# Optimization experiments

Measured on AMD Instinct MI355X. Metric: run time of the kernel, lower is better.

Reference implementation:

```python
import jax, jax.numpy as jnp
import numpy as np

SEQ_LEN, BATCH, IN_SIZE = 512, 1024, 3
HID, HID_FC, OUT = 512, 512, 1
HORIZON = 96


def gru_cell(x, h, w_ih, w_hh, b_ih, b_hh):
    # PyTorch GRU cell math. x: [B, in], h: [B, H], w_ih: [3H, in], w_hh: [3H, H]
    gi = x @ w_ih.T + b_ih
    gh = h @ w_hh.T + b_hh
    i_r, i_z, i_n = jnp.split(gi, 3, axis=-1)
    h_r, h_z, h_n = jnp.split(gh, 3, axis=-1)
    r = jax.nn.sigmoid(i_r + h_r)
    z = jax.nn.sigmoid(i_z + h_z)
    n = jnp.tanh(i_n + r * h_n)
    return (1.0 - z) * n + z * h


def setup_inputs() -> dict:
    key = jax.random.key(0)
    ks = jax.random.split(key, 16)
    s_in = 1.0 / np.sqrt(HID)
    inp = {
        'src': jax.random.normal(ks[0], (SEQ_LEN, BATCH, IN_SIZE), dtype=jnp.float32),
        'enc_wih': jax.random.uniform(ks[1], (3 * HID, IN_SIZE), minval=-s_in, maxval=s_in),
        'enc_whh': jax.random.uniform(ks[2], (3 * HID, HID), minval=-s_in, maxval=s_in),
        'enc_bih': jax.random.uniform(ks[3], (3 * HID,), minval=-s_in, maxval=s_in),
        'enc_bhh': jax.random.uniform(ks[4], (3 * HID,), minval=-s_in, maxval=s_in),
        'dec_wih': jax.random.uniform(ks[5], (3 * HID, OUT), minval=-s_in, maxval=s_in),
        'dec_whh': jax.random.uniform(ks[6], (3 * HID, HID), minval=-s_in, maxval=s_in),
        'dec_bih': jax.random.uniform(ks[7], (3 * HID,), minval=-s_in, maxval=s_in),
        'dec_bhh': jax.random.uniform(ks[8], (3 * HID,), minval=-s_in, maxval=s_in),
        'w1': jax.random.uniform(ks[9], (HID_FC, HID), minval=-s_in, maxval=s_in),
        'b1': jax.random.uniform(ks[10], (HID_FC,), minval=-s_in, maxval=s_in),
        'w2': jax.random.uniform(ks[11], (OUT, HID_FC), minval=-1.0 / np.sqrt(HID_FC), maxval=1.0 / np.sqrt(HID_FC)),
        'b2': jax.random.uniform(ks[12], (OUT,), minval=-1.0 / np.sqrt(HID_FC), maxval=1.0 / np.sqrt(HID_FC)),
        'horizon': HORIZON,
    }
    return inp


def reference(src, enc_wih, enc_whh, enc_bih, enc_bhh,
              dec_wih, dec_whh, dec_bih, dec_bhh,
              w1, b1, w2, b2, horizon):
    B = src.shape[1]
    h0 = jnp.zeros((B, HID), dtype=src.dtype)

    # Encoder: run GRU over time; only final hidden state is used.
    def enc_step(h, x_t):
        return gru_cell(x_t, h, enc_wih, enc_whh, enc_bih, enc_bhh), None
    h, _ = jax.lax.scan(enc_step, h0, src)

    dec_in0 = src[-1, :, 0:1]  # [B, 1]

    def dec_step(carry, _):
        dec_in, h = carry
        h = gru_cell(dec_in, h, dec_wih, dec_whh, dec_bih, dec_bhh)
        y = jax.nn.relu(h @ w1.T + b1) @ w2.T + b2  # [B, 1]
        return (y, h), y
    _, outputs = jax.lax.scan(dec_step, (dec_in0, h), None, length=horizon)
    return outputs  # [horizon, B, 1]
```

## Files before the change

kernel.cpp:

```cpp
#include <hip/hip_runtime.h>

typedef __bf16 bf16x8 __attribute__((ext_vector_type(8)));
typedef float f32x4 __attribute__((ext_vector_type(4)));

#define HID 512
#define BATCH 1024
#define SEQL 512
#define NWG 256
#define NTHR 512

#define OFF_ENH 0u
#define OFF_ENL 1572864u
#define OFF_DEH 3145728u
#define OFF_DEL 4718592u
#define OFF_W1H 6291456u
#define OFF_W1L 6815744u
#define OFF_HP0 7340032u
#define OFF_HP1 9437184u
#define OFF_FC1 11534336u
#define OFF_BAR 13631488u
#define WS_NEED 13635584u

#define LDS_LO 32768
#define SWZ(row, cb) (((row) << 10) + ((cb) ^ (((row) & 7) << 4)))

__device__ __forceinline__ f32x4 mfma16(bf16x8 a, bf16x8 b, f32x4 c) {
  return __builtin_amdgcn_mfma_f32_16x16x32_bf16(a, b, c, 0, 0, 0);
}
__device__ __forceinline__ float sig_(float x) { return 1.0f / (1.0f + __expf(-x)); }
__device__ __forceinline__ float tanh_(float x) { return 1.0f - 2.0f / (__expf(2.0f * x) + 1.0f); }

__device__ __forceinline__ unsigned long long ald64(const void* p) {
  return __hip_atomic_load((const unsigned long long*)p, __ATOMIC_RELAXED,
                           __HIP_MEMORY_SCOPE_AGENT);
}
__device__ __forceinline__ void ast32(void* p, unsigned v) {
  __hip_atomic_store((unsigned*)p, v, __ATOMIC_RELAXED, __HIP_MEMORY_SCOPE_AGENT);
}
__device__ __forceinline__ void astf(void* p, float v) {
  __hip_atomic_store((float*)p, v, __ATOMIC_RELAXED, __HIP_MEMORY_SCOPE_AGENT);
}

__global__ void split_w(const float* __restrict__ a, __bf16* __restrict__ hi,
                        __bf16* __restrict__ lo, int n) {
  int i = blockIdx.x * blockDim.x + threadIdx.x;
  if (i < n) {
    float v = a[i];
    __bf16 h = (__bf16)v;
    hi[i] = h;
    lo[i] = (__bf16)(v - (float)h);
  }
}

__device__ __forceinline__ void gbar(unsigned* cnt, unsigned target) {
  __syncthreads();
  if (threadIdx.x == 0) {
    __hip_atomic_fetch_add(cnt, 1u, __ATOMIC_RELAXED, __HIP_MEMORY_SCOPE_AGENT);
    int i = 0;
    while (__hip_atomic_load(cnt, __ATOMIC_RELAXED, __HIP_MEMORY_SCOPE_AGENT) < target) {
      __builtin_amdgcn_s_sleep(2);
      if (++i >= 30000) break;
    }
  }
  __syncthreads();
  __builtin_amdgcn_sched_barrier(0);
}

__device__ __forceinline__ void stage_h32(char* sm, const unsigned* hsrc, int row0, int tid) {
  const int cp = tid & 255;
  const int rh = (tid >> 8) << 4;
  const unsigned long long* src =
      (const unsigned long long*)hsrc + ((size_t)(row0 + rh) << 8) + cp;
  unsigned long long b[16];
#pragma unroll
  for (int j = 0; j < 16; ++j) b[j] = ald64(src + (size_t)j * 256);
#pragma unroll
  for (int j = 0; j < 16; ++j) {
    const int row = rh + j;
    const unsigned p0 = (unsigned)b[j];
    const unsigned p1 = (unsigned)(b[j] >> 32);
    const unsigned hw = (p0 & 0xffffu) | (p1 << 16);
    const unsigned lw = (p0 >> 16) | (p1 & 0xffff0000u);
    const int sa = SWZ(row, cp << 2);
    *(unsigned*)(sm + sa) = hw;
    *(unsigned*)(sm + LDS_LO + sa) = lw;
  }
}

__device__ __forceinline__ void gh3(const char* sm, int rl, int kbb,
                                    const __bf16* __restrict__ Bh,
                                    const __bf16* __restrict__ Bl,
                                    const int (&boff)[3], f32x4 (&acc)[3]) {
#pragma unroll 4
  for (int kc = 0; kc < 16; ++kc) {
    const int sa = SWZ(rl, (kc << 6) + kbb);
    bf16x8 ah = *(const bf16x8*)(sm + sa);
    bf16x8 al = *(const bf16x8*)(sm + LDS_LO + sa);
    const int ko = kc << 5;
#pragma unroll
    for (int f = 0; f < 3; ++f) {
      bf16x8 bh = *(const bf16x8*)(Bh + boff[f] + ko);
      bf16x8 bl = *(const bf16x8*)(Bl + boff[f] + ko);
      acc[f] = mfma16(ah, bh, acc[f]);
      acc[f] = mfma16(al, bh, acc[f]);
      acc[f] = mfma16(ah, bl, acc[f]);
    }
  }
}

__device__ __forceinline__ void gh1(const char* sm, int rl, int kbb,
                                    const __bf16* __restrict__ Bh,
                                    const __bf16* __restrict__ Bl, int boff, f32x4& acc) {
#pragma unroll 4
  for (int kc = 0; kc < 16; ++kc) {
    const int sa = SWZ(rl, (kc << 6) + kbb);
    bf16x8 ah = *(const bf16x8*)(sm + sa);
    bf16x8 al = *(const bf16x8*)(sm + LDS_LO + sa);
    const int ko = kc << 5;
    bf16x8 bh = *(const bf16x8*)(Bh + boff + ko);
    bf16x8 bl = *(const bf16x8*)(Bl + boff + ko);
    acc = mfma16(ah, bh, acc);
    acc = mfma16(al, bh, acc);
    acc = mfma16(ah, bl, acc);
  }
}

__global__ void __launch_bounds__(NTHR, 2) seq2seq_main(
    const float* __restrict__ src, const float* __restrict__ enc_wih,
    const float* __restrict__ enc_bih, const float* __restrict__ enc_bhh,
    const float* __restrict__ dec_wih, const float* __restrict__ dec_bih,
    const float* __restrict__ dec_bhh, const float* __restrict__ b1,
    const float* __restrict__ w2, const float* __restrict__ b2,
    const int* __restrict__ hor, float* __restrict__ out, char* __restrict__ ws) {
  __shared__ f32x4 smv[4096];
  char* sm = (char*)smv;
  float* yb = (float*)sm;

  const __bf16* ench_hi = (const __bf16*)(ws + OFF_ENH);
  const __bf16* ench_lo = (const __bf16*)(ws + OFF_ENL);
  const __bf16* dech_hi = (const __bf16*)(ws + OFF_DEH);
  const __bf16* dech_lo = (const __bf16*)(ws + OFF_DEL);
  const __bf16* w1h = (const __bf16*)(ws + OFF_W1H);
  const __bf16* w1l = (const __bf16*)(ws + OFF_W1L);
  unsigned* hp0 = (unsigned*)(ws + OFF_HP0);
  unsigned* hp1 = (unsigned*)(ws + OFF_HP1);
  float* fc1 = (float*)(ws + OFF_FC1);

  const int bid = blockIdx.x;
  const int G = bid >> 3;
  const int ct = bid & 7;
  const int tid = threadIdx.x;
  const int wv = tid >> 6;
  const int lane = tid & 63;
  const int lan15 = lane & 15;
  const int crow = (lane >> 4) << 2;
  const int kbe = (lane >> 4) << 3;
  const int kbb = kbe << 1;
  const int wr = wv & 1;
  const int wc = wv >> 1;
  const int rl = (wr << 4) + lan15;
  const int row0 = G << 5;
  const int cg = (ct << 6) + (wc << 4) + lan15;

  unsigned* cnt = (unsigned*)(ws + OFF_BAR) + (G << 5);

  int boff[3];
#pragma unroll
  for (int g = 0; g < 3; ++g) boff[g] = ((g << 9) + cg) * HID + kbe;
  const int boff_fc = cg * HID + kbe;

  float wE[3][3], biE[3], bhE[3];
#pragma unroll
  for (int g = 0; g < 3; ++g) {
    const int j = (g << 9) + cg;
    wE[g][0] = enc_wih[j * 3 + 0];
    wE[g][1] = enc_wih[j * 3 + 1];
    wE[g][2] = enc_wih[j * 3 + 2];
    biE[g] = enc_bih[j];
    bhE[g] = enc_bhh[j];
  }

  const f32x4 zf = {0.0f, 0.0f, 0.0f, 0.0f};
  float hpv[4] = {0.f, 0.f, 0.f, 0.f};

  for (int t = 0; t < SEQL; ++t) {
    f32x4 acc[3];
#pragma unroll
    for (int f = 0; f < 3; ++f) acc[f] = zf;

    if (t != 0) {
      stage_h32(sm, (t & 1) ? hp1 : hp0, row0, tid);
      __syncthreads();
      gh3(sm, rl, kbb, ench_hi, ench_lo, boff, acc);
    }

    unsigned* hn = ((t + 1) & 1) ? hp1 : hp0;
#pragma unroll
    for (int reg = 0; reg < 4; ++reg) {
      const int row = row0 + (wr << 4) + crow + reg;
      const float* xp = src + ((size_t)t * BATCH + row) * 3;
      const float x0 = xp[0], x1 = xp[1], x2 = xp[2];
      const float gir = fmaf(x0, wE[0][0], fmaf(x1, wE[0][1], fmaf(x2, wE[0][2], biE[0])));
      const float giz = fmaf(x0, wE[1][0], fmaf(x1, wE[1][1], fmaf(x2, wE[1][2], biE[1])));
      const float gin = fmaf(x0, wE[2][0], fmaf(x1, wE[2][1], fmaf(x2, wE[2][2], biE[2])));
      const float rg = sig_(gir + acc[0][reg] + bhE[0]);
      const float zg = sig_(giz + acc[1][reg] + bhE[1]);
      const float ng = tanh_(gin + rg * (acc[2][reg] + bhE[2]));
      const float hv = fmaf(zg, hpv[reg] - ng, ng);
      hpv[reg] = hv;
      const __bf16 hb = (__bf16)hv;
      const __bf16 lb = (__bf16)(hv - (float)hb);
      const unsigned pw = (unsigned)__builtin_bit_cast(unsigned short, hb) |
                          ((unsigned)__builtin_bit_cast(unsigned short, lb) << 16);
      ast32(hn + (size_t)row * HID + cg, pw);
    }
    gbar(cnt, 8u * (unsigned)(t + 1));
  }

  float wD[3], biD[3], bhD[3];
#pragma unroll
  for (int g = 0; g < 3; ++g) {
    const int j = (g << 9) + cg;
    wD[g] = dec_wih[j];
    biD[g] = dec_bih[j];
    bhD[g] = dec_bhh[j];
  }
  const float b1c = b1[cg];
  const float b2v = b2[0];
  float w2p0[4], w2p1[4];
#pragma unroll
  for (int j = 0; j < 4; ++j) {
    w2p0[j] = w2[2 * (lane + j * 64)];
    w2p1[j] = w2[2 * (lane + j * 64) + 1];
  }
  int H = hor[0];
  if (H < 1 || H > 96) H = 96;

  for (int t = 0; t < H; ++t) {
    float din[4];
    if (t == 0) {
#pragma unroll
      for (int reg = 0; reg < 4; ++reg) {
        const int row = row0 + (wr << 4) + crow + reg;
        din[reg] = src[((size_t)(SEQL - 1) * BATCH + row) * 3];
      }
    } else {
#pragma unroll
      for (int rr = 0; rr < 4; ++rr) {
        const int row = row0 + (wv << 2) + rr;
        const unsigned long long* fp = (const unsigned long long*)fc1 + ((size_t)row << 8);
        float s = 0.0f;
#pragma unroll
        for (int j = 0; j < 4; ++j) {
          const unsigned long long w = ald64(fp + lane + (j << 6));
          const float f0 = __builtin_bit_cast(float, (unsigned)(w & 0xffffffffULL));
          const float f1 = __builtin_bit_cast(float, (unsigned)(w >> 32));
          s = fmaf(f0, w2p0[j], fmaf(f1, w2p1[j], s));
        }
#pragma unroll
        for (int off = 1; off < 64; off <<= 1) s += __shfl_xor(s, off, 64);
        if (lane == 0) yb[(wv << 2) + rr] = s + b2v;
      }
      __syncthreads();
      if (ct == 0 && tid < 32) out[(size_t)(t - 1) * BATCH + row0 + tid] = yb[tid];
#pragma unroll
      for (int reg = 0; reg < 4; ++reg) din[reg] = yb[(wr << 4) + crow + reg];
      __syncthreads();
    }

    {
      stage_h32(sm, (t & 1) ? hp1 : hp0, row0, tid);
      __syncthreads();
      f32x4 acc[3];
#pragma unroll
      for (int f = 0; f < 3; ++f) acc[f] = zf;
      gh3(sm, rl, kbb, dech_hi, dech_lo, boff, acc);

      unsigned* hn = ((t + 1) & 1) ? hp1 : hp0;
#pragma unroll
      for (int reg = 0; reg < 4; ++reg) {
        const int row = row0 + (wr << 4) + crow + reg;
        const float d = din[reg];
        const float rg = sig_(fmaf(d, wD[0], biD[0]) + acc[0][reg] + bhD[0]);
        const float zg = sig_(fmaf(d, wD[1], biD[1]) + acc[1][reg] + bhD[1]);
        const float ng = tanh_(fmaf(d, wD[2], biD[2]) + rg * (acc[2][reg] + bhD[2]));
        const float hv = fmaf(zg, hpv[reg] - ng, ng);
        hpv[reg] = hv;
        const __bf16 hb = (__bf16)hv;
        const __bf16 lb = (__bf16)(hv - (float)hb);
        const unsigned pw = (unsigned)__builtin_bit_cast(unsigned short, hb) |
                            ((unsigned)__builtin_bit_cast(unsigned short, lb) << 16);
        ast32(hn + (size_t)row * HID + cg, pw);
      }
    }
    gbar(cnt, 8u * (unsigned)(SEQL + 2 * t + 1));

    {
      stage_h32(sm, ((t + 1) & 1) ? hp1 : hp0, row0, tid);
      __syncthreads();
      f32x4 fa = zf;
      gh1(sm, rl, kbb, w1h, w1l, boff_fc, fa);
#pragma unroll
      for (int reg = 0; reg < 4; ++reg) {
        const int row = row0 + (wr << 4) + crow + reg;
        astf(&fc1[(size_t)row * HID + cg], fmaxf(fa[reg] + b1c, 0.0f));
      }
    }
    gbar(cnt, 8u * (unsigned)(SEQL + 2 * t + 2));
  }

  if (ct == 0) {
#pragma unroll
    for (int rr = 0; rr < 4; ++rr) {
      const int row = row0 + (wv << 2) + rr;
      const unsigned long long* fp = (const unsigned long long*)fc1 + ((size_t)row << 8);
      float s = 0.0f;
#pragma unroll
      for (int j = 0; j < 4; ++j) {
        const unsigned long long w = ald64(fp + lane + (j << 6));
        const float f0 = __builtin_bit_cast(float, (unsigned)(w & 0xffffffffULL));
        const float f1 = __builtin_bit_cast(float, (unsigned)(w >> 32));
        s = fmaf(f0, w2p0[j], fmaf(f1, w2p1[j], s));
      }
#pragma unroll
      for (int off = 1; off < 64; off <<= 1) s += __shfl_xor(s, off, 64);
      if (lane == 0) yb[(wv << 2) + rr] = s + b2v;
    }
    __syncthreads();
    if (tid < 32) out[(size_t)(H - 1) * BATCH + row0 + tid] = yb[tid];
  }
}

extern "C" void kernel_launch(void* const* d_in, const int* in_sizes, int n_in,
                              void* d_out, int out_size, void* d_ws, size_t ws_size,
                              hipStream_t stream) {
  if (ws_size < WS_NEED) return;

  const float* src = (const float*)d_in[0];
  const float* enc_wih = (const float*)d_in[1];
  const float* enc_whh = (const float*)d_in[2];
  const float* enc_bih = (const float*)d_in[3];
  const float* enc_bhh = (const float*)d_in[4];
  const float* dec_wih = (const float*)d_in[5];
  const float* dec_whh = (const float*)d_in[6];
  const float* dec_bih = (const float*)d_in[7];
  const float* dec_bhh = (const float*)d_in[8];
  const float* w1 = (const float*)d_in[9];
  const float* b1 = (const float*)d_in[10];
  const float* w2 = (const float*)d_in[11];
  const float* b2 = (const float*)d_in[12];
  const int* hor = (const int*)d_in[13];
  float* out = (float*)d_out;
  char* ws = (char*)d_ws;

  hipMemsetAsync(ws + OFF_BAR, 0, 4096, stream);

  split_w<<<dim3(3072), dim3(256), 0, stream>>>(enc_whh, (__bf16*)(ws + OFF_ENH),
                                                (__bf16*)(ws + OFF_ENL), 786432);
  split_w<<<dim3(3072), dim3(256), 0, stream>>>(dec_whh, (__bf16*)(ws + OFF_DEH),
                                                (__bf16*)(ws + OFF_DEL), 786432);
  split_w<<<dim3(1024), dim3(256), 0, stream>>>(w1, (__bf16*)(ws + OFF_W1H),
                                                (__bf16*)(ws + OFF_W1L), 262144);

  void* args[] = {&src, &enc_wih, &enc_bih, &enc_bhh, &dec_wih, &dec_bih, &dec_bhh,
                  &b1, &w2, &b2, &hor, &out, &ws};
  hipLaunchCooperativeKernel((void*)seq2seq_main, dim3(NWG), dim3(NTHR), args, 0, stream);
}
```

Before: 16.29 ms.

## Assign row groups and column tiles per XCD so barrier groups share an XCD

At kernel start, each workgroup reads its hardware XCD id and claims a slot from a per-XCD counter. The slot sets the (column tile, row group) pair, so that the 8 column tiles of one row group and its per-group barrier land on the same XCD and keep L2 locality for the h exchange. Workgroups that do not get a slot fall back to a CAS search over unclaimed pairs. A grid-wide wait with a timeout sits between the two phases. The encoder also issues its src input loads before the h staging and MFMA work so their latency overlaps. The change adds startup atomics and a spin, and relies on XCC_ID placement.

```diff
diff --git a/kernel.cpp b/kernel.cpp
--- a/kernel.cpp
+++ b/kernel.cpp
@@ -19,7 +19,8 @@
 #define OFF_HP1 9437184u
 #define OFF_FC1 11534336u
 #define OFF_BAR 13631488u
-#define WS_NEED 13635584u
+#define OFF_ASN 13635584u
+#define WS_NEED 13639680u
 
 #define LDS_LO 32768
 #define SWZ(row, cb) (((row) << 10) + ((cb) ^ (((row) & 7) << 4)))
@@ -135,6 +136,7 @@
   __shared__ f32x4 smv[4096];
   char* sm = (char*)smv;
   float* yb = (float*)sm;
+  int* s_pair = (int*)sm;
 
   const __bf16* ench_hi = (const __bf16*)(ws + OFF_ENH);
   const __bf16* ench_lo = (const __bf16*)(ws + OFF_ENL);
@@ -145,11 +147,53 @@
   unsigned* hp0 = (unsigned*)(ws + OFF_HP0);
   unsigned* hp1 = (unsigned*)(ws + OFF_HP1);
   float* fc1 = (float*)(ws + OFF_FC1);
+  unsigned* xcd_cnt = (unsigned*)(ws + OFF_ASN);
+  unsigned* root = (unsigned*)(ws + OFF_ASN + 512);
+  unsigned* taken = (unsigned*)(ws + OFF_ASN + 1024);
 
   const int bid = blockIdx.x;
-  const int G = bid >> 3;
-  const int ct = bid & 7;
   const int tid = threadIdx.x;
+
+  if (tid == 0) {
+    int xcd;
+    asm volatile("s_getreg_b32 %0, hwreg(HW_REG_XCC_ID)" : "=s"(xcd));
+    xcd &= 7;
+    const unsigned slot = __hip_atomic_fetch_add(&xcd_cnt[xcd * 16], 1u, __ATOMIC_RELAXED,
+                                                 __HIP_MEMORY_SCOPE_AGENT);
+    int p = -1;
+    if (slot < 32u) {
+      p = xcd * 32 + (int)slot;
+      __hip_atomic_store(&taken[p], 1u, __ATOMIC_RELAXED, __HIP_MEMORY_SCOPE_AGENT);
+    }
+    __hip_atomic_fetch_add(root, 1u, __ATOMIC_RELEASE, __HIP_MEMORY_SCOPE_AGENT);
+    int i = 0;
+    while (__hip_atomic_load(root, __ATOMIC_ACQUIRE, __HIP_MEMORY_SCOPE_AGENT) < NWG) {
+      __builtin_amdgcn_s_sleep(2);
+      if (++i >= 30000) break;
+    }
+    if (p < 0) {
+      for (int k = 0; k < 256; ++k) {
+        const int j = (bid + k) & 255;
+        if (__hip_atomic_load(&taken[j], __ATOMIC_RELAXED, __HIP_MEMORY_SCOPE_AGENT) == 0u) {
+          unsigned exp = 0u;
+          if (__hip_atomic_compare_exchange_strong(&taken[j], &exp, 1u, __ATOMIC_ACQ_REL,
+                                                   __ATOMIC_RELAXED,
+                                                   __HIP_MEMORY_SCOPE_AGENT)) {
+            p = j;
+            break;
+          }
+        }
+      }
+    }
+    if (p < 0) p = ((bid & 7) << 5) | (bid >> 3);
+    *s_pair = p;
+  }
+  __syncthreads();
+  const int pr = *s_pair;
+  __syncthreads();
+  const int ct = pr >> 5;
+  const int G = pr & 31;
+
   const int wv = tid >> 6;
   const int lane = tid & 63;
   const int lan15 = lane & 15;
@@ -184,6 +228,16 @@
   float hpv[4] = {0.f, 0.f, 0.f, 0.f};
 
   for (int t = 0; t < SEQL; ++t) {
+    float xv[4][3];
+#pragma unroll
+    for (int reg = 0; reg < 4; ++reg) {
+      const int row = row0 + (wr << 4) + crow + reg;
+      const float* xp = src + ((size_t)t * BATCH + row) * 3;
+      xv[reg][0] = xp[0];
+      xv[reg][1] = xp[1];
+      xv[reg][2] = xp[2];
+    }
+
     f32x4 acc[3];
 #pragma unroll
     for (int f = 0; f < 3; ++f) acc[f] = zf;
@@ -198,8 +252,7 @@
 #pragma unroll
     for (int reg = 0; reg < 4; ++reg) {
       const int row = row0 + (wr << 4) + crow + reg;
-      const float* xp = src + ((size_t)t * BATCH + row) * 3;
-      const float x0 = xp[0], x1 = xp[1], x2 = xp[2];
+      const float x0 = xv[reg][0], x1 = xv[reg][1], x2 = xv[reg][2];
       const float gir = fmaf(x0, wE[0][0], fmaf(x1, wE[0][1], fmaf(x2, wE[0][2], biE[0])));
       const float giz = fmaf(x0, wE[1][0], fmaf(x1, wE[1][1], fmaf(x2, wE[1][2], biE[1])));
       const float gin = fmaf(x0, wE[2][0], fmaf(x1, wE[2][1], fmaf(x2, wE[2][2], biE[2])));
@@ -353,7 +406,7 @@
   float* out = (float*)d_out;
   char* ws = (char*)d_ws;
 
-  hipMemsetAsync(ws + OFF_BAR, 0, 4096, stream);
+  hipMemsetAsync(ws + OFF_BAR, 0, 8192, stream);
 
   split_w<<<dim3(3072), dim3(256), 0, stream>>>(enc_whh, (__bf16*)(ws + OFF_ENH),
                                                 (__bf16*)(ws + OFF_ENL), 786432);
```

Measured after the change: 16.02 ms. About the same (-1.7%).

## Split work across 512 smaller workgroups of 16 batch rows each

Applied to the files above, without the earlier changes.

Changes the persistent grid from 256 workgroups of 512 threads handling 32 batch rows each to 512 workgroups of 256 threads handling 16 rows, halving LDS staging per group and raising occupancy bounds. It also hoists the per-step input loads ahead of the recurrent matmul so their latency overlaps it. The cooperative launch is replaced with a plain launch, so co-residency of all 512 groups for the spin barrier is no longer guaranteed and the barrier has a timeout break. Each group now redundantly streams the full weight slices for half as many rows, doubling weight reads per row.

```diff
diff --git a/kernel.cpp b/kernel.cpp
--- a/kernel.cpp
+++ b/kernel.cpp
@@ -6,8 +6,8 @@
 #define HID 512
 #define BATCH 1024
 #define SEQL 512
-#define NWG 256
-#define NTHR 512
+#define NWG 512
+#define NTHR 256
 
 #define OFF_ENH 0u
 #define OFF_ENL 1572864u
@@ -19,9 +19,9 @@
 #define OFF_HP1 9437184u
 #define OFF_FC1 11534336u
 #define OFF_BAR 13631488u
-#define WS_NEED 13635584u
-
-#define LDS_LO 32768
+#define WS_NEED 13639680u
+
+#define LDS_LO 16384
 #define SWZ(row, cb) (((row) << 10) + ((cb) ^ (((row) & 7) << 4)))
 
 __device__ __forceinline__ f32x4 mfma16(bf16x8 a, bf16x8 b, f32x4 c) {
@@ -66,22 +66,18 @@
   __builtin_amdgcn_sched_barrier(0);
 }
 
-__device__ __forceinline__ void stage_h32(char* sm, const unsigned* hsrc, int row0, int tid) {
-  const int cp = tid & 255;
-  const int rh = (tid >> 8) << 4;
-  const unsigned long long* src =
-      (const unsigned long long*)hsrc + ((size_t)(row0 + rh) << 8) + cp;
+__device__ __forceinline__ void stage_h16(char* sm, const unsigned* hsrc, int row0, int tid) {
+  const unsigned long long* src = (const unsigned long long*)hsrc + ((size_t)row0 << 8) + tid;
   unsigned long long b[16];
 #pragma unroll
   for (int j = 0; j < 16; ++j) b[j] = ald64(src + (size_t)j * 256);
 #pragma unroll
   for (int j = 0; j < 16; ++j) {
-    const int row = rh + j;
     const unsigned p0 = (unsigned)b[j];
     const unsigned p1 = (unsigned)(b[j] >> 32);
     const unsigned hw = (p0 & 0xffffu) | (p1 << 16);
     const unsigned lw = (p0 >> 16) | (p1 & 0xffff0000u);
-    const int sa = SWZ(row, cp << 2);
+    const int sa = SWZ(j, tid << 2);
     *(unsigned*)(sm + sa) = hw;
     *(unsigned*)(sm + LDS_LO + sa) = lw;
   }
@@ -125,14 +121,14 @@
   }
 }
 
-__global__ void __launch_bounds__(NTHR, 2) seq2seq_main(
+__global__ void __launch_bounds__(NTHR, 4) seq2seq_main(
     const float* __restrict__ src, const float* __restrict__ enc_wih,
     const float* __restrict__ enc_bih, const float* __restrict__ enc_bhh,
     const float* __restrict__ dec_wih, const float* __restrict__ dec_bih,
     const float* __restrict__ dec_bhh, const float* __restrict__ b1,
     const float* __restrict__ w2, const float* __restrict__ b2,
     const int* __restrict__ hor, float* __restrict__ out, char* __restrict__ ws) {
-  __shared__ f32x4 smv[4096];
+  __shared__ f32x4 smv[2048];
   char* sm = (char*)smv;
   float* yb = (float*)sm;
 
@@ -156,11 +152,9 @@
   const int crow = (lane >> 4) << 2;
   const int kbe = (lane >> 4) << 3;
   const int kbb = kbe << 1;
-  const int wr = wv & 1;
-  const int wc = wv >> 1;
-  const int rl = (wr << 4) + lan15;
-  const int row0 = G << 5;
-  const int cg = (ct << 6) + (wc << 4) + lan15;
+  const int rl = lan15;
+  const int row0 = G << 4;
+  const int cg = (ct << 6) + (wv << 4) + lan15;
 
   unsigned* cnt = (unsigned*)(ws + OFF_BAR) + (G << 5);
 
@@ -184,12 +178,22 @@
   float hpv[4] = {0.f, 0.f, 0.f, 0.f};
 
   for (int t = 0; t < SEQL; ++t) {
+    float xv[4][3];
+#pragma unroll
+    for (int reg = 0; reg < 4; ++reg) {
+      const int row = row0 + crow + reg;
+      const float* xp = src + ((size_t)t * BATCH + row) * 3;
+      xv[reg][0] = xp[0];
+      xv[reg][1] = xp[1];
+      xv[reg][2] = xp[2];
+    }
+
     f32x4 acc[3];
 #pragma unroll
     for (int f = 0; f < 3; ++f) acc[f] = zf;
 
     if (t != 0) {
-      stage_h32(sm, (t & 1) ? hp1 : hp0, row0, tid);
+      stage_h16(sm, (t & 1) ? hp1 : hp0, row0, tid);
       __syncthreads();
       gh3(sm, rl, kbb, ench_hi, ench_lo, boff, acc);
     }
@@ -197,9 +201,8 @@
     unsigned* hn = ((t + 1) & 1) ? hp1 : hp0;
 #pragma unroll
     for (int reg = 0; reg < 4; ++reg) {
-      const int row = row0 + (wr << 4) + crow + reg;
-      const float* xp = src + ((size_t)t * BATCH + row) * 3;
-      const float x0 = xp[0], x1 = xp[1], x2 = xp[2];
+      const int row = row0 + crow + reg;
+      const float x0 = xv[reg][0], x1 = xv[reg][1], x2 = xv[reg][2];
       const float gir = fmaf(x0, wE[0][0], fmaf(x1, wE[0][1], fmaf(x2, wE[0][2], biE[0])));
       const float giz = fmaf(x0, wE[1][0], fmaf(x1, wE[1][1], fmaf(x2, wE[1][2], biE[1])));
       const float gin = fmaf(x0, wE[2][0], fmaf(x1, wE[2][1], fmaf(x2, wE[2][2], biE[2])));
@@ -241,7 +244,7 @@
     if (t == 0) {
 #pragma unroll
       for (int reg = 0; reg < 4; ++reg) {
-        const int row = row0 + (wr << 4) + crow + reg;
+        const int row = row0 + crow + reg;
         din[reg] = src[((size_t)(SEQL - 1) * BATCH + row) * 3];
       }
     } else {
@@ -262,14 +265,14 @@
         if (lane == 0) yb[(wv << 2) + rr] = s + b2v;
       }
       __syncthreads();
-      if (ct == 0 && tid < 32) out[(size_t)(t - 1) * BATCH + row0 + tid] = yb[tid];
-#pragma unroll
-      for (int reg = 0; reg < 4; ++reg) din[reg] = yb[(wr << 4) + crow + reg];
+      if (ct == 0 && tid < 16) out[(size_t)(t - 1) * BATCH + row0 + tid] = yb[tid];
+#pragma unroll
+      for (int reg = 0; reg < 4; ++reg) din[reg] = yb[crow + reg];
       __syncthreads();
     }
 
     {
-      stage_h32(sm, (t & 1) ? hp1 : hp0, row0, tid);
+      stage_h16(sm, (t & 1) ? hp1 : hp0, row0, tid);
       __syncthreads();
       f32x4 acc[3];
 #pragma unroll
@@ -279,7 +282,7 @@
       unsigned* hn = ((t + 1) & 1) ? hp1 : hp0;
 #pragma unroll
       for (int reg = 0; reg < 4; ++reg) {
-        const int row = row0 + (wr << 4) + crow + reg;
+        const int row = row0 + crow + reg;
         const float d = din[reg];
         const float rg = sig_(fmaf(d, wD[0], biD[0]) + acc[0][reg] + bhD[0]);
         const float zg = sig_(fmaf(d, wD[1], biD[1]) + acc[1][reg] + bhD[1]);
@@ -296,13 +299,13 @@
     gbar(cnt, 8u * (unsigned)(SEQL + 2 * t + 1));
 
     {
-      stage_h32(sm, ((t + 1) & 1) ? hp1 : hp0, row0, tid);
+      stage_h16(sm, ((t + 1) & 1) ? hp1 : hp0, row0, tid);
       __syncthreads();
       f32x4 fa = zf;
       gh1(sm, rl, kbb, w1h, w1l, boff_fc, fa);
 #pragma unroll
       for (int reg = 0; reg < 4; ++reg) {
-        const int row = row0 + (wr << 4) + crow + reg;
+        const int row = row0 + crow + reg;
         astf(&fc1[(size_t)row * HID + cg], fmaxf(fa[reg] + b1c, 0.0f));
       }
     }
@@ -327,7 +330,7 @@
       if (lane == 0) yb[(wv << 2) + rr] = s + b2v;
     }
     __syncthreads();
-    if (tid < 32) out[(size_t)(H - 1) * BATCH + row0 + tid] = yb[tid];
+    if (tid < 16) out[(size_t)(H - 1) * BATCH + row0 + tid] = yb[tid];
   }
 }
 
@@ -353,7 +356,7 @@
   float* out = (float*)d_out;
   char* ws = (char*)d_ws;
 
-  hipMemsetAsync(ws + OFF_BAR, 0, 4096, stream);
+  hipMemsetAsync(ws + OFF_BAR, 0, 8192, stream);
 
   split_w<<<dim3(3072), dim3(256), 0, stream>>>(enc_whh, (__bf16*)(ws + OFF_ENH),
                                                 (__bf16*)(ws + OFF_ENL), 786432);
@@ -362,7 +365,6 @@
   split_w<<<dim3(1024), dim3(256), 0, stream>>>(w1, (__bf16*)(ws + OFF_W1H),
                                                 (__bf16*)(ws + OFF_W1L), 262144);
 
-  void* args[] = {&src, &enc_wih, &enc_bih, &enc_bhh, &dec_wih, &dec_bih, &dec_bhh,
-                  &b1, &w2, &b2, &hor, &out, &ws};
-  hipLaunchCooperativeKernel((void*)seq2seq_main, dim3(NWG), dim3(NTHR), args, 0, stream);
-}
+  seq2seq_main<<<dim3(NWG), dim3(NTHR), 0, stream>>>(
+      src, enc_wih, enc_bih, enc_bhh, dec_wih, dec_bih, dec_bhh, b1, w2, b2, hor, out, ws);
+}
```

Result: faster. 15.33 ms (-5.9%).
